# Kernel optimization log

Hardware: AMD Instinct MI355X
Metric: run time of the kernel (lower is better)

Reference implementation:

```python
import jax, jax.numpy as jnp
import numpy as np

B, NB, K, S = 4, 131072, 32, 768


def setup_inputs() -> dict:
    key = jax.random.key(0)
    k1, k2, k3, k4 = jax.random.split(key, 4)
    N = B * NB
    logits_embedding = jax.random.normal(k1, (N, 4), dtype=jnp.float32)
    logits_seediness = jax.random.normal(k2, (N, 1), dtype=jnp.float32)
    coords = jax.random.uniform(k3, (N, 3), dtype=jnp.float32, minval=0.0, maxval=float(S))
    inst = jax.random.randint(k4, (N,), 0, K).astype(jnp.float32)
    batch = jnp.repeat(jnp.arange(B, dtype=jnp.float32), NB)
    labels = jnp.concatenate(
        [batch[:, None], coords, jnp.zeros((N, 1), jnp.float32), inst[:, None]], axis=1)
    return {"logits_embedding": logits_embedding,
            "logits_seediness": logits_seediness,
            "labels": labels}


def reference(logits_embedding, logits_seediness, labels):
    half = S / 2.0
    # coords_embedding = emb[:, :3] + (voxel_coords - S/2) / (S/2)
    ce = logits_embedding[:, :3] + (labels[:, 1:4] - half) / half          # [N,3]
    sigma = logits_embedding[:, 3]                                          # [N]
    seed = logits_seediness.reshape(-1)                                     # [N]
    inst = labels[:, 5].astype(jnp.int32)                                   # [N]

    # batch ids are contiguous by construction -> reshape to [B, NB, ...]
    ce = ce.reshape(B, NB, 3)
    sigma = sigma.reshape(B, NB)
    seed = seed.reshape(B, NB)
    inst = inst.reshape(B, NB)

    onehot = (inst[:, :, None] == jnp.arange(K)[None, None, :]).astype(jnp.float32)  # [B,NB,K]
    counts = jnp.maximum(onehot.sum(axis=1), 1.0)                                    # [B,K]

    centers = jnp.einsum('bnk,bnd->bkd', onehot, ce) / counts[:, :, None]            # [B,K,3]
    sigmas = jnp.einsum('bnk,bn->bk', onehot, sigma) / counts                        # [B,K]

    # squared distance of every point to every instance center
    diff = ce[:, :, None, :] - centers[:, None, :, :]                                # [B,NB,K,3]
    dist2 = jnp.sum(diff * diff, axis=-1)                                            # [B,NB,K]

    arg = jnp.clip(dist2 / (2.0 * sigmas[:, None, :] ** 2), 1e-7, 100.0)
    p = jnp.exp(-arg)                                                                # [B,NB,K]

    # mask loss: log(p) == -arg exactly
    mask_loss = -(onehot * (-arg) + (1.0 - onehot) * jnp.log1p(-p)).sum(axis=(1, 2)) / NB / K  # [B]

    smooth = (onehot * jnp.abs(sigma[:, :, None] - sigmas[:, None, :])).sum(axis=1) / counts
    smooth_loss = smooth.sum(axis=1) / K                                             # [B]

    seed_term = (onehot * (seed[:, :, None] - p) ** 2).sum(axis=1) / counts
    seed_loss = seed_term.sum(axis=1) / K                                            # [B]

    # inter-cluster hinge, sum over unordered pairs i<j, denom K*(K-1)
    cdiff = centers[:, :, None, :] - centers[:, None, :, :]                          # [B,K,K,3]
    cd2 = jnp.sum(cdiff * cdiff, axis=-1)
    eye = jnp.eye(K, dtype=jnp.float32)[None]
    d = jnp.sqrt(jnp.where(eye > 0, 1.0, cd2))                                       # safe sqrt on diag
    hinge = jnp.maximum(0.0, 2.0 * 0.5 - d) ** 2 * (1.0 - eye)
    inter_loss = hinge.sum(axis=(1, 2)) / 2.0 / (K * (K - 1))                        # [B]

    loss = jnp.mean(mask_loss + smooth_loss + inter_loss + seed_loss)

    # accuracy: assign each point to nearest center (instance ids are 0..K-1)
    pred = jnp.argmin(dist2, axis=2)                                                 # [B,NB]
    acc = jnp.mean((pred == inst).astype(jnp.float32))
    return loss, jax.lax.stop_gradient(acc)
```

## Files before the change

### kernel.cpp

```cpp
#include <hip/hip_runtime.h>

#define B_ 4
#define NB_ 131072
#define K_ 32
#define N_ (B_*NB_)
#define BK_ (B_*K_)
#define NACC 256
#define ABLK 64
#define PTS_PER_ACC 2048

#define ACC_OFF  0
#define FIN_OFF  (NACC*5*K_)
#define PART_OFF (FIN_OFF + 6*BK_)

__global__ __launch_bounds__(256) void k_accum(
    const float4* __restrict__ emb, const float* __restrict__ labels,
    float* __restrict__ ws)
{
    __shared__ float sacc[5*K_];
    int tid = threadIdx.x;
    if (tid < 5*K_) sacc[tid] = 0.f;
    __syncthreads();
    int start = blockIdx.x * PTS_PER_ACC;
    #pragma unroll
    for (int i = 0; i < PTS_PER_ACC/256; ++i) {
        int n = start + i*256 + tid;
        float4 e = emb[n];
        const float* lr = labels + (size_t)n*6;
        float c1 = lr[1], c2 = lr[2], c3 = lr[3];
        int inst = ((int)lr[5]) & 31;
        float cex = e.x + (c1 - 384.f)/384.f;
        float cey = e.y + (c2 - 384.f)/384.f;
        float cez = e.z + (c3 - 384.f)/384.f;
        atomicAdd(&sacc[0*K_+inst], cex);
        atomicAdd(&sacc[1*K_+inst], cey);
        atomicAdd(&sacc[2*K_+inst], cez);
        atomicAdd(&sacc[3*K_+inst], e.w);
        atomicAdd(&sacc[4*K_+inst], 1.0f);
    }
    __syncthreads();
    if (tid < 5*K_) ws[ACC_OFF + blockIdx.x*5*K_ + tid] = sacc[tid];
}

__global__ __launch_bounds__(128) void k_finalize(float* __restrict__ ws)
{
    int t = threadIdx.x;
    int b = t >> 5, k = t & 31;
    float a0=0.f,a1=0.f,a2=0.f,a3=0.f,a4=0.f;
    for (int j = 0; j < ABLK; ++j) {
        const float* rp = ws + ACC_OFF + (size_t)(b*ABLK + j)*5*K_;
        a0 += rp[0*K_+k]; a1 += rp[1*K_+k]; a2 += rp[2*K_+k];
        a3 += rp[3*K_+k]; a4 += rp[4*K_+k];
    }
    float cnt = fmaxf(a4, 1.0f);
    float inv = 1.0f / cnt;
    float sg = a3 / cnt;
    float* fin = ws + FIN_OFF;
    fin[0*BK_+t] = a0 / cnt;
    fin[1*BK_+t] = a1 / cnt;
    fin[2*BK_+t] = a2 / cnt;
    fin[3*BK_+t] = sg;
    fin[4*BK_+t] = inv;
    fin[5*BK_+t] = 1.0f / (2.0f*sg*sg);
}

__global__ __launch_bounds__(256) void k_main(
    const float4* __restrict__ emb, const float* __restrict__ seedp,
    const float* __restrict__ labels, const float* __restrict__ ws,
    float4* __restrict__ part)
{
    __shared__ float s_cx[K_], s_cy[K_], s_cz[K_], s_sig[K_], s_inv[K_], s_i2s[K_];
    int tid = threadIdx.x;
    int n = blockIdx.x * 256 + tid;
    int b = blockIdx.x >> 9;
    const float* fin = ws + FIN_OFF;
    if (tid < K_) {
        int idx = b*K_ + tid;
        s_cx[tid]  = fin[0*BK_+idx];
        s_cy[tid]  = fin[1*BK_+idx];
        s_cz[tid]  = fin[2*BK_+idx];
        s_sig[tid] = fin[3*BK_+idx];
        s_inv[tid] = fin[4*BK_+idx];
        s_i2s[tid] = fin[5*BK_+idx];
    }
    __syncthreads();
    float4 e = emb[n];
    const float* lr = labels + (size_t)n*6;
    float c1 = lr[1], c2 = lr[2], c3 = lr[3];
    int inst = ((int)lr[5]) & 31;
    float sd = seedp[n];
    float cex = e.x + (c1 - 384.f)/384.f;
    float cey = e.y + (c2 - 384.f)/384.f;
    float cez = e.z + (c3 - 384.f)/384.f;
    float sigma = e.w;
    float best = 3.4e38f; int bi = 0;
    float msum = 0.f, p_in = 0.f, sig_in = 0.f, inv_in = 0.f;
    #pragma unroll
    for (int k = 0; k < K_; ++k) {
        float dx = cex - s_cx[k];
        float dy = cey - s_cy[k];
        float dz = cez - s_cz[k];
        float d2 = dx*dx + dy*dy + dz*dz;
        if (d2 < best) { best = d2; bi = k; }
        float arg = d2 * s_i2s[k];
        arg = fminf(fmaxf(arg, 1e-7f), 100.f);
        float p = __expf(-arg);
        bool isin = (k == inst);
        float l1p = __logf(1.0f - p);
        msum += isin ? (-arg) : l1p;
        if (isin) { p_in = p; sig_in = s_sig[k]; inv_in = s_inv[k]; }
    }
    float smoothv = fabsf(sigma - sig_in) * inv_in;
    float dsd = sd - p_in;
    float seedv = dsd*dsd*inv_in;
    float accv = (bi == inst) ? 1.0f : 0.0f;

    float v0 = msum, v1 = smoothv, v2 = seedv, v3 = accv;
    for (int off = 32; off; off >>= 1) {
        v0 += __shfl_down(v0, off);
        v1 += __shfl_down(v1, off);
        v2 += __shfl_down(v2, off);
        v3 += __shfl_down(v3, off);
    }
    __shared__ float sred[4][4];
    int wid = tid >> 6, lane = tid & 63;
    if (lane == 0) { sred[wid][0]=v0; sred[wid][1]=v1; sred[wid][2]=v2; sred[wid][3]=v3; }
    __syncthreads();
    if (tid == 0) {
        float r0=0.f,r1=0.f,r2=0.f,r3=0.f;
        for (int w = 0; w < 4; ++w) { r0+=sred[w][0]; r1+=sred[w][1]; r2+=sred[w][2]; r3+=sred[w][3]; }
        part[blockIdx.x] = make_float4(r0, r1, r2, r3);
    }
}

__global__ __launch_bounds__(256) void k_final(
    const float* __restrict__ ws, const float* __restrict__ part,
    float* __restrict__ out)
{
    int tid = threadIdx.x;

    int pair = tid >> 4;
    int lane16 = tid & 15;
    int f = pair >> 2, b = pair & 3;
    float v = 0.f;
    #pragma unroll
    for (int j = 0; j < 32; ++j) {
        int blk = b*512 + lane16*32 + j;
        v += part[blk*4 + f];
    }
    v += __shfl_down(v, 8);
    v += __shfl_down(v, 4);
    v += __shfl_down(v, 2);
    v += __shfl_down(v, 1);
    __shared__ float S[16];
    if (lane16 == 0) S[pair] = v;

    float h = 0.f;
    for (int idx = tid; idx < B_*K_*K_; idx += 256) {
        int bb = idx >> 10;
        int ij = idx & 1023;
        int i = ij >> 5, j = ij & 31;
        if (i != j) {
            const float* fin = ws + FIN_OFF;
            float dx = fin[0*BK_ + bb*K_+i] - fin[0*BK_ + bb*K_+j];
            float dy = fin[1*BK_ + bb*K_+i] - fin[1*BK_ + bb*K_+j];
            float dz = fin[2*BK_ + bb*K_+i] - fin[2*BK_ + bb*K_+j];
            float cd2 = dx*dx + dy*dy + dz*dz;
            float d = sqrtf(cd2);
            float hg = fmaxf(0.f, 1.0f - d);
            h += hg*hg;
        }
    }
    for (int off = 32; off; off >>= 1) h += __shfl_down(h, off);
    __shared__ float sh[4];
    int wid = tid >> 6, lane = tid & 63;
    if (lane == 0) sh[wid] = h;
    __syncthreads();

    if (tid == 0) {
        float ht = sh[0]+sh[1]+sh[2]+sh[3];
        float loss = 0.f;
        for (int bb = 0; bb < B_; ++bb) {
            float mask_l   = -S[0*4+bb] / (float)NB_ / (float)K_;
            float smooth_l =  S[1*4+bb] / (float)K_;
            float seed_l   =  S[2*4+bb] / (float)K_;
            loss += mask_l + smooth_l + seed_l;
        }
        loss = loss / (float)B_ + ht / (2.0f * (float)(K_*(K_-1)) * (float)B_);
        float acc = (S[3*4+0]+S[3*4+1]+S[3*4+2]+S[3*4+3]) / (float)N_;
        out[0] = loss;
        out[1] = acc;
    }
}

extern "C" void kernel_launch(void* const* d_in, const int* in_sizes, int n_in,
                              void* d_out, int out_size, void* d_ws, size_t ws_size,
                              hipStream_t stream)
{
    const float4* emb    = (const float4*)d_in[0];
    const float*  seedp  = (const float*)d_in[1];
    const float*  labels = (const float*)d_in[2];
    float* ws  = (float*)d_ws;
    float* out = (float*)d_out;

    k_accum   <<<NACC,   256, 0, stream>>>(emb, labels, ws);
    k_finalize<<<1,      128, 0, stream>>>(ws);
    k_main    <<<N_/256, 256, 0, stream>>>(emb, seedp, labels, ws,
                                           (float4*)(ws + PART_OFF));
    k_final   <<<1,      256, 0, stream>>>(ws, ws + PART_OFF, out);
}
```

Before: 50.84 us.

## Fuse finalize into main kernel, skip negligible log terms, pack argmin

Removes the single-block finalize launch: every k_main block now reduces the 64 per-block accumulator rows for its batch itself, computes the centers and sigmas in shared memory, and the first block of each batch writes them out for k_final. The inner loop over 32 centers packs distance and index into one unsigned min for the argmin, and skips exp/log with a wavefront-wide vote when every arg is at least 15, where log(1-p) is negligible. The in-instance term is computed once outside the loop. k_accum goes to 1024-thread blocks and uses float2 loads for coords. This adds redundant accumulator reads per block and a small approximation in the mask loss.

```diff
diff --git a/kernel.cpp b/kernel.cpp
--- a/kernel.cpp
+++ b/kernel.cpp
@@ -13,7 +13,7 @@
 #define FIN_OFF  (NACC*5*K_)
 #define PART_OFF (FIN_OFF + 6*BK_)
 
-__global__ __launch_bounds__(256) void k_accum(
+__global__ __launch_bounds__(1024) void k_accum(
     const float4* __restrict__ emb, const float* __restrict__ labels,
     float* __restrict__ ws)
 {
@@ -23,15 +23,16 @@
     __syncthreads();
     int start = blockIdx.x * PTS_PER_ACC;
     #pragma unroll
-    for (int i = 0; i < PTS_PER_ACC/256; ++i) {
-        int n = start + i*256 + tid;
+    for (int i = 0; i < PTS_PER_ACC/1024; ++i) {
+        int n = start + i*1024 + tid;
         float4 e = emb[n];
         const float* lr = labels + (size_t)n*6;
-        float c1 = lr[1], c2 = lr[2], c3 = lr[3];
+        float c1 = lr[1];
+        float2 c23 = *reinterpret_cast<const float2*>(lr + 2);
         int inst = ((int)lr[5]) & 31;
-        float cex = e.x + (c1 - 384.f)/384.f;
-        float cey = e.y + (c2 - 384.f)/384.f;
-        float cez = e.z + (c3 - 384.f)/384.f;
+        float cex = e.x + (c1    - 384.f)/384.f;
+        float cey = e.y + (c23.x - 384.f)/384.f;
+        float cez = e.z + (c23.y - 384.f)/384.f;
         atomicAdd(&sacc[0*K_+inst], cex);
         atomicAdd(&sacc[1*K_+inst], cey);
         atomicAdd(&sacc[2*K_+inst], cez);
@@ -42,76 +43,95 @@
     if (tid < 5*K_) ws[ACC_OFF + blockIdx.x*5*K_ + tid] = sacc[tid];
 }
 
-__global__ __launch_bounds__(128) void k_finalize(float* __restrict__ ws)
-{
-    int t = threadIdx.x;
-    int b = t >> 5, k = t & 31;
-    float a0=0.f,a1=0.f,a2=0.f,a3=0.f,a4=0.f;
-    for (int j = 0; j < ABLK; ++j) {
-        const float* rp = ws + ACC_OFF + (size_t)(b*ABLK + j)*5*K_;
-        a0 += rp[0*K_+k]; a1 += rp[1*K_+k]; a2 += rp[2*K_+k];
-        a3 += rp[3*K_+k]; a4 += rp[4*K_+k];
-    }
-    float cnt = fmaxf(a4, 1.0f);
-    float inv = 1.0f / cnt;
-    float sg = a3 / cnt;
-    float* fin = ws + FIN_OFF;
-    fin[0*BK_+t] = a0 / cnt;
-    fin[1*BK_+t] = a1 / cnt;
-    fin[2*BK_+t] = a2 / cnt;
-    fin[3*BK_+t] = sg;
-    fin[4*BK_+t] = inv;
-    fin[5*BK_+t] = 1.0f / (2.0f*sg*sg);
-}
-
 __global__ __launch_bounds__(256) void k_main(
     const float4* __restrict__ emb, const float* __restrict__ seedp,
-    const float* __restrict__ labels, const float* __restrict__ ws,
+    const float* __restrict__ labels, float* __restrict__ ws,
     float4* __restrict__ part)
 {
-    __shared__ float s_cx[K_], s_cy[K_], s_cz[K_], s_sig[K_], s_inv[K_], s_i2s[K_];
+    __shared__ float s_raw[5*K_];
+    __shared__ float s_fin[6*K_];
     int tid = threadIdx.x;
     int n = blockIdx.x * 256 + tid;
     int b = blockIdx.x >> 9;
-    const float* fin = ws + FIN_OFF;
+
+    if (tid < 5*K_) {
+        float a = 0.f;
+        const float* base = ws + ACC_OFF + (size_t)b*ABLK*5*K_ + tid;
+        #pragma unroll 8
+        for (int j = 0; j < ABLK; ++j) a += base[(size_t)j*5*K_];
+        s_raw[tid] = a;
+    }
+    __syncthreads();
     if (tid < K_) {
-        int idx = b*K_ + tid;
-        s_cx[tid]  = fin[0*BK_+idx];
-        s_cy[tid]  = fin[1*BK_+idx];
-        s_cz[tid]  = fin[2*BK_+idx];
-        s_sig[tid] = fin[3*BK_+idx];
-        s_inv[tid] = fin[4*BK_+idx];
-        s_i2s[tid] = fin[5*BK_+idx];
-    }
-    __syncthreads();
+        float cnt = fmaxf(s_raw[4*K_+tid], 1.f);
+        float inv = 1.f / cnt;
+        float cx = s_raw[0*K_+tid] * inv;
+        float cy = s_raw[1*K_+tid] * inv;
+        float cz = s_raw[2*K_+tid] * inv;
+        float sg = s_raw[3*K_+tid] * inv;
+        float i2s = 1.f / (2.f*sg*sg);
+        s_fin[0*K_+tid] = cx;
+        s_fin[1*K_+tid] = cy;
+        s_fin[2*K_+tid] = cz;
+        s_fin[3*K_+tid] = sg;
+        s_fin[4*K_+tid] = inv;
+        s_fin[5*K_+tid] = i2s;
+        if ((blockIdx.x & 511) == 0) {
+            float* fin = ws + FIN_OFF;
+            fin[0*BK_ + b*K_+tid] = cx;
+            fin[1*BK_ + b*K_+tid] = cy;
+            fin[2*BK_ + b*K_+tid] = cz;
+            fin[3*BK_ + b*K_+tid] = sg;
+            fin[4*BK_ + b*K_+tid] = inv;
+            fin[5*BK_ + b*K_+tid] = i2s;
+        }
+    }
+    __syncthreads();
+
     float4 e = emb[n];
     const float* lr = labels + (size_t)n*6;
-    float c1 = lr[1], c2 = lr[2], c3 = lr[3];
+    float c1 = lr[1];
+    float2 c23 = *reinterpret_cast<const float2*>(lr + 2);
     int inst = ((int)lr[5]) & 31;
     float sd = seedp[n];
-    float cex = e.x + (c1 - 384.f)/384.f;
-    float cey = e.y + (c2 - 384.f)/384.f;
-    float cez = e.z + (c3 - 384.f)/384.f;
+    float cex = e.x + (c1    - 384.f)/384.f;
+    float cey = e.y + (c23.x - 384.f)/384.f;
+    float cez = e.z + (c23.y - 384.f)/384.f;
     float sigma = e.w;
-    float best = 3.4e38f; int bi = 0;
-    float msum = 0.f, p_in = 0.f, sig_in = 0.f, inv_in = 0.f;
+
+    unsigned bestpk = 0xffffffffu;
+    float msum = 0.f;
     #pragma unroll
     for (int k = 0; k < K_; ++k) {
-        float dx = cex - s_cx[k];
-        float dy = cey - s_cy[k];
-        float dz = cez - s_cz[k];
+        float dx = cex - s_fin[0*K_+k];
+        float dy = cey - s_fin[1*K_+k];
+        float dz = cez - s_fin[2*K_+k];
         float d2 = dx*dx + dy*dy + dz*dz;
-        if (d2 < best) { best = d2; bi = k; }
-        float arg = d2 * s_i2s[k];
-        arg = fminf(fmaxf(arg, 1e-7f), 100.f);
-        float p = __expf(-arg);
-        bool isin = (k == inst);
-        float l1p = __logf(1.0f - p);
-        msum += isin ? (-arg) : l1p;
-        if (isin) { p_in = p; sig_in = s_sig[k]; inv_in = s_inv[k]; }
-    }
-    float smoothv = fabsf(sigma - sig_in) * inv_in;
-    float dsd = sd - p_in;
+        unsigned pk = (__float_as_uint(d2) & ~31u) | (unsigned)k;
+        bestpk = min(bestpk, pk);
+        float arg = d2 * s_fin[5*K_+k];
+        if (__any(arg < 15.f)) {
+            float argc = fminf(fmaxf(arg, 1e-7f), 100.f);
+            float p = __expf(-argc);
+            float l1p = __logf(1.f - p);
+            msum += (arg < 15.f) ? l1p : 0.f;
+        }
+    }
+    int bi = (int)(bestpk & 31u);
+
+    float dxI = cex - s_fin[0*K_+inst];
+    float dyI = cey - s_fin[1*K_+inst];
+    float dzI = cez - s_fin[2*K_+inst];
+    float d2I = dxI*dxI + dyI*dyI + dzI*dzI;
+    float argRawI = d2I * s_fin[5*K_+inst];
+    float argI = fminf(fmaxf(argRawI, 1e-7f), 100.f);
+    float pI = __expf(-argI);
+    if (argRawI < 15.f) msum -= __logf(1.f - pI);
+    msum -= argI;
+
+    float inv_in = s_fin[4*K_+inst];
+    float smoothv = fabsf(sigma - s_fin[3*K_+inst]) * inv_in;
+    float dsd = sd - pI;
     float seedv = dsd*dsd*inv_in;
     float accv = (bi == inst) ? 1.0f : 0.0f;
 
@@ -203,9 +223,8 @@
     float* ws  = (float*)d_ws;
     float* out = (float*)d_out;
 
-    k_accum   <<<NACC,   256, 0, stream>>>(emb, labels, ws);
-    k_finalize<<<1,      128, 0, stream>>>(ws);
-    k_main    <<<N_/256, 256, 0, stream>>>(emb, seedp, labels, ws,
+    k_accum <<<NACC,    1024, 0, stream>>>(emb, labels, ws);
+    k_main  <<<N_/256,  256,  0, stream>>>(emb, seedp, labels, ws,
                                            (float4*)(ws + PART_OFF));
-    k_final   <<<1,      256, 0, stream>>>(ws, ws + PART_OFF, out);
-}
+    k_final <<<1,       256,  0, stream>>>(ws, ws + PART_OFF, out);
+}
```

After: 42.69 us. -16.0%, faster.
